# Performance work log

Hardware: AMD Instinct MI355X
Metric: run time of the kernel (lower is better)

## Reference

```python
import jax, jax.numpy as jnp
import numpy as np
import math

D, NH, NL, NP_ = 256, 8, 3, 4
BS, LQ = 32, 300
SHAPES = [(80, 80), (40, 40), (20, 20)]
LV = sum(h * w for h, w in SHAPES)  # 8400
DFF = 1024


def _offset_bias():
    # faithful to MSDeformableAttention._reset_parameters
    thetas = jnp.arange(NH, dtype=jnp.float32) * (2.0 * math.pi / NH)
    grid = jnp.stack([jnp.cos(thetas), jnp.sin(thetas)], -1)
    grid = grid / jnp.abs(grid).max(-1, keepdims=True)
    grid = jnp.tile(grid.reshape(NH, 1, 1, 2), (1, NL, NP_, 1))
    grid = grid * jnp.arange(1, NP_ + 1, dtype=jnp.float32).reshape(1, 1, -1, 1)
    return grid.reshape(-1)


def setup_inputs() -> dict:
    key = jax.random.key(0)
    ks = iter(jax.random.split(key, 64))
    rn = lambda shape, s=0.02: jax.random.normal(next(ks), shape, jnp.float32) * s
    z = lambda n: jnp.zeros((n,), jnp.float32)
    o = lambda n: jnp.ones((n,), jnp.float32)
    inp = {
        'tgt': jax.random.normal(next(ks), (BS, LQ, D), jnp.float32),
        'reference_points': jax.random.uniform(next(ks), (BS, LQ, NL, 2), jnp.float32),
        'memory': jax.random.normal(next(ks), (BS, LV, D), jnp.float32),
        'query_pos_embed': jax.random.normal(next(ks), (BS, LQ, D), jnp.float32),
        'memory_spatial_shapes': np.array(SHAPES, dtype=np.int64),
        'memory_level_start_index': np.array([0, 6400, 8000], dtype=np.int64),
        # self-attn
        'Wq': rn((D, D)), 'bq': z(D), 'Wk': rn((D, D)), 'bk': z(D),
        'Wv': rn((D, D)), 'bv': z(D), 'Wo': rn((D, D)), 'bo': z(D),
        'ln1_g': o(D), 'ln1_b': z(D),
        # deformable cross-attn
        'W_vproj': rn((D, D)), 'b_vproj': z(D),
        'W_off': rn((D, NH * NL * NP_ * 2), 0.001), 'b_off': _offset_bias(),
        'W_attn': rn((D, NH * NL * NP_)), 'b_attn': z(NH * NL * NP_),
        'W_out': rn((D, D)), 'b_out': z(D),
        'ln2_g': o(D), 'ln2_b': z(D),
        # FFN
        'W1': rn((D, DFF)), 'b1': z(DFF), 'W2': rn((DFF, D)), 'b2': z(D),
        'ln3_g': o(D), 'ln3_b': z(D),
    }
    return inp


def _ln(x, g, b):
    m = x.mean(-1, keepdims=True)
    v = ((x - m) ** 2).mean(-1, keepdims=True)
    return (x - m) / jnp.sqrt(v + 1e-5) * g + b


def _ms_deform(value, shapes, loc, aw):
    # value [bs,Lv,nh,c]; loc [bs,Lq,nh,NL,NP,2] in [0,1]; aw [bs,Lq,nh,NL,NP]
    bs, Lv, nh, c = value.shape
    Lq = loc.shape[1]
    npts = loc.shape[4]
    grids = 2.0 * loc - 1.0
    out = jnp.zeros((bs, nh, Lq, c), value.dtype)
    start = 0
    for lvl, (h, w) in enumerate(shapes):
        flat = value[:, start:start + h * w].transpose(0, 2, 1, 3)  # [bs,nh,hw,c]
        start += h * w
        g = grids[:, :, :, lvl].transpose(0, 2, 1, 3, 4).reshape(bs, nh, Lq * npts, 2)
        # align_corners=False pixel coords
        x = (g[..., 0] + 1.0) * (w / 2.0) - 0.5
        y = (g[..., 1] + 1.0) * (h / 2.0) - 0.5
        x0 = jnp.floor(x); y0 = jnp.floor(y)
        wx1 = x - x0; wy1 = y - y0
        samp = jnp.zeros((bs, nh, Lq * npts, c), value.dtype)
        for xi, yi, wgt in ((x0, y0, (1 - wx1) * (1 - wy1)),
                            (x0 + 1, y0, wx1 * (1 - wy1)),
                            (x0, y0 + 1, (1 - wx1) * wy1),
                            (x0 + 1, y0 + 1, wx1 * wy1)):
            valid = (xi >= 0) & (xi < w) & (yi >= 0) & (yi < h)
            idx = (jnp.clip(yi, 0, h - 1) * w + jnp.clip(xi, 0, w - 1)).astype(jnp.int32)
            idx = jnp.broadcast_to(idx[..., None], idx.shape + (c,))
            gv = jnp.take_along_axis(flat, idx, axis=2)  # [bs,nh,Lq*np,c]
            samp = samp + gv * (wgt * valid.astype(value.dtype))[..., None]
        samp = samp.reshape(bs, nh, Lq, npts, c)
        a = aw[:, :, :, lvl].transpose(0, 2, 1, 3)  # [bs,nh,Lq,np]
        out = out + (samp * a[..., None]).sum(3)
    return out.transpose(0, 2, 1, 3).reshape(bs, Lq, nh * c)


def reference(tgt, reference_points, memory, query_pos_embed,
              memory_spatial_shapes, memory_level_start_index,
              Wq, bq, Wk, bk, Wv, bv, Wo, bo, ln1_g, ln1_b,
              W_vproj, b_vproj, W_off, b_off, W_attn, b_attn, W_out, b_out,
              ln2_g, ln2_b, W1, b1, W2, b2, ln3_g, ln3_b):
    shapes = [(int(h), int(w)) for h, w in np.asarray(memory_spatial_shapes)]
    bs, Lq, d = tgt.shape
    hd = d // NH
    # --- self attention (dropout=eval identity, attn_mask=None) ---
    q = tgt + query_pos_embed
    qh = (q @ Wq + bq).reshape(bs, Lq, NH, hd)
    kh = (q @ Wk + bk).reshape(bs, Lq, NH, hd)
    vh = (tgt @ Wv + bv).reshape(bs, Lq, NH, hd)
    att = jax.nn.softmax(jnp.einsum('bqhd,bkhd->bhqk', qh, kh) / jnp.sqrt(jnp.float32(hd)), axis=-1)
    sa = jnp.einsum('bhqk,bkhd->bqhd', att, vh).reshape(bs, Lq, d) @ Wo + bo
    tgt = _ln(tgt + sa, ln1_g, ln1_b)
    # --- deformable cross attention ---
    qc = tgt + query_pos_embed
    value = (memory @ W_vproj + b_vproj).reshape(bs, -1, NH, hd)
    off = (qc @ W_off + b_off).reshape(bs, Lq, NH, NL, NP_, 2)
    aw = jax.nn.softmax((qc @ W_attn + b_attn).reshape(bs, Lq, NH, NL * NP_), axis=-1)
    aw = aw.reshape(bs, Lq, NH, NL, NP_)
    norm = jnp.array([[w, h] for h, w in shapes], jnp.float32)  # flip -> (w,h)
    loc = reference_points[:, :, None, :, None, :] + off / norm[None, None, None, :, None, :]
    ca = _ms_deform(value, shapes, loc, aw) @ W_out + b_out
    tgt = _ln(tgt + ca, ln2_g, ln2_b)
    # --- FFN ---
    h = jax.nn.relu(tgt @ W1 + b1) @ W2 + b2
    return _ln(tgt + h, ln3_g, ln3_b)
```

## Files before the change

### kernel.cpp

```cpp
#include <hip/hip_runtime.h>
#include <hip/hip_bf16.h>

#define D_      256
#define NH_     8
#define HD_     32
#define NL_     3
#define NP_4    4
#define BS_     32
#define LQ_     300
#define LV_     8400
#define DFF_    1024
#define NTOK    (BS_ * LQ_)
#define NVAL    (BS_ * LV_)

typedef __attribute__((ext_vector_type(8))) short bf16x8;
typedef __attribute__((ext_vector_type(4))) float f32x4;

__device__ inline unsigned short f2bf(float x) {
    union { float f; unsigned u; } v; v.f = x;
    unsigned r = v.u + 0x7FFFu + ((v.u >> 16) & 1u);
    return (unsigned short)(r >> 16);
}
__device__ inline float bf2f(unsigned short x) {
    union { unsigned u; float f; } v; v.u = ((unsigned)x) << 16;
    return v.f;
}

struct TrDesc { const float* W; unsigned short* Wt; int K; int N; };
struct TrPack { TrDesc d[10]; };

__global__ __launch_bounds__(256)
void tr_kernel(TrPack p) {
    TrDesc d = p.d[blockIdx.z];
    const int n0 = blockIdx.x * 32, k0 = blockIdx.y * 32;
    if (n0 >= d.N || k0 >= d.K) return;
    __shared__ float t[32][33];
    const int tx = threadIdx.x & 31, ty = threadIdx.x >> 5;
    #pragma unroll
    for (int i = 0; i < 4; ++i) {
        int k = k0 + ty + i * 8, n = n0 + tx;
        t[ty + i * 8][tx] = (k < d.K && n < d.N) ? d.W[(size_t)k * d.N + n] : 0.f;
    }
    __syncthreads();
    #pragma unroll
    for (int i = 0; i < 4; ++i) {
        int n = n0 + ty + i * 8, k = k0 + tx;
        if (n < d.N && k < d.K) d.Wt[(size_t)n * d.K + k] = f2bf(t[tx][ty + i * 8]);
    }
}

template <int AROWS, int KK, int TC, int AMODE, int CMODE>
__global__ __launch_bounds__(256, 2)
void gemm_wreg(const void* __restrict__ Ain, const float* __restrict__ A2,
               const unsigned short* __restrict__ Wt, const float* __restrict__ bias,
               void* __restrict__ Cout, int M, int N) {
    constexpr int KSTEPS = KK / 32;
    constexpr int RT = AROWS / 16;
    constexpr int LDK = KK + 8;
    constexpr int TPR = 256 / AROWS;
    constexpr int KSEG = KK / TPR;
    __shared__ unsigned short Alds[AROWS * LDK];

    const int tid = threadIdx.x;
    const int lane = tid & 63, w = tid >> 6;
    const int quad = lane >> 4, l16 = lane & 15;
    const int rowBase = blockIdx.y * AROWS;
    const int colW = blockIdx.x * (4 * TC * 16) + w * (TC * 16);

    bf16x8 wf[TC][KSTEPS];
    #pragma unroll
    for (int j = 0; j < TC; ++j) {
        int col = colW + j * 16 + l16;
        if (col > N - 1) col = N - 1;
        const unsigned short* wp = Wt + (size_t)col * KK;
        #pragma unroll
        for (int s = 0; s < KSTEPS; ++s)
            wf[j][s] = *(const bf16x8*)(wp + s * 32 + quad * 8);
    }

    {
        const int row = tid / TPR;
        const int ks = (tid % TPR) * KSEG;
        const size_t gbase = (size_t)(rowBase + row) * KK + ks;
        unsigned short* dst = &Alds[row * LDK + ks];
        if (AMODE == 2) {
            const int4* ap = (const int4*)((const unsigned short*)Ain + gbase);
            int4 wa[KSEG / 8];
            #pragma unroll
            for (int j = 0; j < KSEG / 8; ++j) wa[j] = ap[j];
            #pragma unroll
            for (int j = 0; j < KSEG / 8; ++j) *(int4*)(dst + j * 8) = wa[j];
        } else {
            const float4* ap = (const float4*)((const float*)Ain + gbase);
            float4 va[KSEG / 4];
            #pragma unroll
            for (int j = 0; j < KSEG / 4; ++j) va[j] = ap[j];
            if (AMODE == 1) {
                const float4* bp = (const float4*)(A2 + gbase);
                float4 vb[KSEG / 4];
                #pragma unroll
                for (int j = 0; j < KSEG / 4; ++j) vb[j] = bp[j];
                #pragma unroll
                for (int j = 0; j < KSEG / 4; ++j) {
                    va[j].x += vb[j].x; va[j].y += vb[j].y;
                    va[j].z += vb[j].z; va[j].w += vb[j].w;
                }
            }
            #pragma unroll
            for (int j = 0; j < KSEG / 4; ++j) {
                ushort4 s4;
                s4.x = f2bf(va[j].x); s4.y = f2bf(va[j].y);
                s4.z = f2bf(va[j].z); s4.w = f2bf(va[j].w);
                *(ushort4*)(dst + j * 4) = s4;
            }
        }
    }
    __syncthreads();

    f32x4 acc[RT][TC];
    #pragma unroll
    for (int rt = 0; rt < RT; ++rt)
        #pragma unroll
        for (int j = 0; j < TC; ++j)
            #pragma unroll
            for (int r = 0; r < 4; ++r) acc[rt][j][r] = 0.f;

    #pragma unroll
    for (int s = 0; s < KSTEPS; ++s) {
        bf16x8 af[RT];
        #pragma unroll
        for (int rt = 0; rt < RT; ++rt)
            af[rt] = *(const bf16x8*)&Alds[(rt * 16 + l16) * LDK + s * 32 + quad * 8];
        #pragma unroll
        for (int rt = 0; rt < RT; ++rt)
            #pragma unroll
            for (int j = 0; j < TC; ++j)
                acc[rt][j] = __builtin_amdgcn_mfma_f32_16x16x32_bf16(af[rt], wf[j][s], acc[rt][j], 0, 0, 0);
    }

    #pragma unroll
    for (int rt = 0; rt < RT; ++rt) {
        #pragma unroll
        for (int j = 0; j < TC; ++j) {
            int col = colW + j * 16 + l16;
            if (col >= N) continue;
            float bb = bias[col];
            #pragma unroll
            for (int r = 0; r < 4; ++r) {
                int row = rowBase + rt * 16 + quad * 4 + r;
                float c = acc[rt][j][r] + bb;
                if (CMODE == 1 || CMODE == 3) c = fmaxf(c, 0.f);
                if (CMODE >= 2)
                    ((unsigned short*)Cout)[(size_t)row * N + col] = f2bf(c);
                else
                    ((float*)Cout)[(size_t)row * N + col] = c;
            }
        }
    }
}

#define PS_STRIDE 344
__global__ __launch_bounds__(256)
void attn_mfma(const unsigned short* __restrict__ qh,
               const unsigned short* __restrict__ kh,
               const unsigned short* __restrict__ vh,
               float* __restrict__ out) {
    __shared__ unsigned short Ps[4 * 16 * PS_STRIDE];
    __shared__ unsigned short Vs[32 * PS_STRIDE];
    const int tid = threadIdx.x;
    const int bh = blockIdx.x >> 1, half_ = blockIdx.x & 1;
    const int b = bh >> 3, h = bh & 7;
    const int w = tid >> 6, lane = tid & 63;
    const int quad = lane >> 4, l16 = lane & 15;

    for (int i = tid; i < 4 * 16 * PS_STRIDE / 2; i += 256) ((unsigned*)Ps)[i] = 0u;

    const size_t hbase = ((size_t)b * LQ_) * D_ + h * HD_;
    for (int it = 0; it < 10; ++it) {
        int chunk = tid + 256 * it;
        int key = chunk >> 3, cc = (chunk & 7) * 4;
        ushort4 v = make_ushort4(0, 0, 0, 0);
        if (key < LQ_) v = *(const ushort4*)(vh + hbase + (size_t)key * D_ + cc);
        Vs[(cc + 0) * PS_STRIDE + key] = v.x;
        Vs[(cc + 1) * PS_STRIDE + key] = v.y;
        Vs[(cc + 2) * PS_STRIDE + key] = v.z;
        Vs[(cc + 3) * PS_STRIDE + key] = v.w;
    }
    __syncthreads();

    const unsigned short* qb = qh + hbase;
    const unsigned short* kb = kh + hbase;
    const float scale = 0.17677669529663687f;

    for (int qt = 10 * half_ + w; qt < 10 * half_ + 10 && qt < 19; qt += 4) {
        int rowq = qt * 16 + l16; if (rowq > LQ_ - 1) rowq = LQ_ - 1;
        bf16x8 aq = *(const bf16x8*)(qb + (size_t)rowq * D_ + quad * 8);

        f32x4 S[19];
        #pragma unroll
        for (int kt = 0; kt < 19; ++kt) {
            int rowk = kt * 16 + l16; if (rowk > LQ_ - 1) rowk = LQ_ - 1;
            bf16x8 bk = *(const bf16x8*)(kb + (size_t)rowk * D_ + quad * 8);
            f32x4 z; z[0] = z[1] = z[2] = z[3] = 0.f;
            S[kt] = __builtin_amdgcn_mfma_f32_16x16x32_bf16(aq, bk, z, 0, 0, 0);
        }
        float mrow[4] = {-1e30f, -1e30f, -1e30f, -1e30f};
        #pragma unroll
        for (int kt = 0; kt < 19; ++kt) {
            bool masked = (kt == 18) && (l16 >= 12);
            #pragma unroll
            for (int r = 0; r < 4; ++r) {
                float s = masked ? -1e30f : S[kt][r] * scale;
                S[kt][r] = s;
                mrow[r] = fmaxf(mrow[r], s);
            }
        }
        #pragma unroll
        for (int r = 0; r < 4; ++r)
            #pragma unroll
            for (int off = 1; off < 16; off <<= 1)
                mrow[r] = fmaxf(mrow[r], __shfl_xor(mrow[r], off));
        float psum[4] = {0.f, 0.f, 0.f, 0.f};
        #pragma unroll
        for (int kt = 0; kt < 19; ++kt)
            #pragma unroll
            for (int r = 0; r < 4; ++r) {
                float p = __expf(S[kt][r] - mrow[r]);
                S[kt][r] = p;
                psum[r] += p;
            }
        #pragma unroll
        for (int r = 0; r < 4; ++r)
            #pragma unroll
            for (int off = 1; off < 16; off <<= 1)
                psum[r] += __shfl_xor(psum[r], off);
        float linv[4];
        #pragma unroll
        for (int r = 0; r < 4; ++r) linv[r] = 1.f / psum[r];

        unsigned short* pw = Ps + w * (16 * PS_STRIDE);
        #pragma unroll
        for (int kt = 0; kt < 19; ++kt)
            #pragma unroll
            for (int r = 0; r < 4; ++r)
                pw[(quad * 4 + r) * PS_STRIDE + kt * 16 + l16] = f2bf(S[kt][r]);

        f32x4 o0, o1;
        #pragma unroll
        for (int r = 0; r < 4; ++r) { o0[r] = 0.f; o1[r] = 0.f; }
        #pragma unroll
        for (int ks = 0; ks < 10; ++ks) {
            bf16x8 ap = *(const bf16x8*)(pw + l16 * PS_STRIDE + ks * 32 + quad * 8);
            bf16x8 b0 = *(const bf16x8*)(Vs + l16 * PS_STRIDE + ks * 32 + quad * 8);
            bf16x8 b1 = *(const bf16x8*)(Vs + (16 + l16) * PS_STRIDE + ks * 32 + quad * 8);
            o0 = __builtin_amdgcn_mfma_f32_16x16x32_bf16(ap, b0, o0, 0, 0, 0);
            o1 = __builtin_amdgcn_mfma_f32_16x16x32_bf16(ap, b1, o1, 0, 0, 0);
        }
        #pragma unroll
        for (int r = 0; r < 4; ++r) {
            int q = qt * 16 + quad * 4 + r;
            if (q < LQ_) {
                size_t ob = ((size_t)b * LQ_ + q) * D_ + h * HD_;
                out[ob + l16]      = o0[r] * linv[r];
                out[ob + 16 + l16] = o1[r] * linv[r];
            }
        }
    }
}

__global__ __launch_bounds__(256)
void ln_kernel(const float* __restrict__ x, const float* __restrict__ r,
               const float* __restrict__ g, const float* __restrict__ bta,
               float* __restrict__ out) {
    const int tok = blockIdx.x;
    const int t = threadIdx.x;
    float v = x[(size_t)tok * D_ + t] + r[(size_t)tok * D_ + t];

    float s = v;
    #pragma unroll
    for (int i = 1; i < 64; i <<= 1) s += __shfl_xor(s, i);
    __shared__ float red1[4];
    if ((t & 63) == 0) red1[t >> 6] = s;
    __syncthreads();
    float mean = (red1[0] + red1[1] + red1[2] + red1[3]) * (1.0f / D_);

    float d = v - mean;
    float s2 = d * d;
    #pragma unroll
    for (int i = 1; i < 64; i <<= 1) s2 += __shfl_xor(s2, i);
    __shared__ float red2[4];
    if ((t & 63) == 0) red2[t >> 6] = s2;
    __syncthreads();
    float var = (red2[0] + red2[1] + red2[2] + red2[3]) * (1.0f / D_);

    out[(size_t)tok * D_ + t] = d * rsqrtf(var + 1e-5f) * g[t] + bta[t];
}

__global__ __launch_bounds__(256)
void deform_kernel(const unsigned short* __restrict__ value,
                   const float* __restrict__ off,
                   const float* __restrict__ awl,
                   const float* __restrict__ ref,
                   float* __restrict__ out) {
    const int lvl_hw[3]    = {80, 40, 20};
    const int lvl_start[3] = {0, 6400, 8000};
    const int gid = blockIdx.x * 16 + (threadIdx.x >> 4);
    const int c2  = (threadIdx.x & 15) * 2;
    const int h   = gid & 7;
    const int bq  = gid >> 3;
    const int b   = bq / LQ_;

    float lg[12];
    const float* ap = awl + (size_t)bq * 96 + h * 12;
    float m = -1e30f;
    #pragma unroll
    for (int j = 0; j < 12; ++j) { lg[j] = ap[j]; m = fmaxf(m, lg[j]); }
    float s = 0.f;
    #pragma unroll
    for (int j = 0; j < 12; ++j) { lg[j] = __expf(lg[j] - m); s += lg[j]; }
    const float inv = 1.0f / s;

    const float* op = off + (size_t)bq * 192 + h * 24;
    const float* rp = ref + (size_t)bq * 6;

    float accx = 0.f, accy = 0.f;
    #pragma unroll
    for (int l = 0; l < NL_; ++l) {
        const int W = lvl_hw[l], H = lvl_hw[l];
        const float fw = (float)W, fh = (float)H;
        const float rx = rp[l * 2 + 0], ry = rp[l * 2 + 1];
        const unsigned short* vbase =
            value + ((size_t)b * LV_ + lvl_start[l]) * D_ + h * HD_ + c2;
        #pragma unroll
        for (int p = 0; p < NP_4; ++p) {
            float ox = op[(l * 4 + p) * 2 + 0], oy = op[(l * 4 + p) * 2 + 1];
            float x = (rx + ox / fw) * fw - 0.5f;
            float y = (ry + oy / fh) * fh - 0.5f;
            float x0f = floorf(x), y0f = floorf(y);
            float wx = x - x0f, wy = y - y0f;
            int x0 = (int)x0f, y0 = (int)y0f;
            float a = lg[l * 4 + p] * inv;
            const float cw[4] = {a * (1.f - wx) * (1.f - wy), a * wx * (1.f - wy),
                                 a * (1.f - wx) * wy,         a * wx * wy};
            const int cx[4] = {x0, x0 + 1, x0,     x0 + 1};
            const int cy[4] = {y0, y0,     y0 + 1, y0 + 1};
            #pragma unroll
            for (int cor = 0; cor < 4; ++cor) {
                int xi = cx[cor], yi = cy[cor];
                if (xi < 0 || xi >= W || yi < 0 || yi >= H) continue;
                unsigned v = *(const unsigned*)(vbase + (size_t)(yi * W + xi) * D_);
                accx += cw[cor] * bf2f((unsigned short)(v & 0xFFFFu));
                accy += cw[cor] * bf2f((unsigned short)(v >> 16));
            }
        }
    }
    float2 o2; o2.x = accx; o2.y = accy;
    *(float2*)(out + (size_t)bq * D_ + h * HD_ + c2) = o2;
}

extern "C" void kernel_launch(void* const* d_in, const int* in_sizes, int n_in,
                              void* d_out, int out_size, void* d_ws, size_t ws_size,
                              hipStream_t stream) {
    const float* tgt   = (const float*)d_in[0];
    const float* refpt = (const float*)d_in[1];
    const float* mem   = (const float*)d_in[2];
    const float* qpos  = (const float*)d_in[3];
    const float* Wq = (const float*)d_in[6],  *bq = (const float*)d_in[7];
    const float* Wk = (const float*)d_in[8],  *bk = (const float*)d_in[9];
    const float* Wv = (const float*)d_in[10], *bv = (const float*)d_in[11];
    const float* Wo = (const float*)d_in[12], *bo = (const float*)d_in[13];
    const float* ln1_g = (const float*)d_in[14], *ln1_b = (const float*)d_in[15];
    const float* W_vproj = (const float*)d_in[16], *b_vproj = (const float*)d_in[17];
    const float* W_off  = (const float*)d_in[18], *b_off  = (const float*)d_in[19];
    const float* W_attn = (const float*)d_in[20], *b_attn = (const float*)d_in[21];
    const float* W_out  = (const float*)d_in[22], *b_out  = (const float*)d_in[23];
    const float* ln2_g = (const float*)d_in[24], *ln2_b = (const float*)d_in[25];
    const float* W1 = (const float*)d_in[26], *b1 = (const float*)d_in[27];
    const float* W2 = (const float*)d_in[28], *b2 = (const float*)d_in[29];
    const float* ln3_g = (const float*)d_in[30], *ln3_b = (const float*)d_in[31];
    float* out = (float*)d_out;

    char* p = (char*)d_ws;
    const size_t TOKD = (size_t)NTOK * D_;
    float* buf_attn = (float*)p; p += TOKD * 4;
    float* buf_tmp  = (float*)p; p += TOKD * 4;
    float* buf_t1   = (float*)p; p += TOKD * 4;
    float* buf_t2   = (float*)p; p += TOKD * 4;
    unsigned short* buf_qh = (unsigned short*)p; p += TOKD * 2;
    unsigned short* buf_kh = (unsigned short*)p; p += TOKD * 2;
    unsigned short* buf_vh = (unsigned short*)p; p += TOKD * 2;
    float* buf_off  = (float*)p; p += (size_t)NTOK * 192 * 4;
    float* buf_awl  = (float*)p; p += (size_t)NTOK * 96 * 4;
    unsigned short* wt_q   = (unsigned short*)p; p += 65536 * 2;
    unsigned short* wt_k   = (unsigned short*)p; p += 65536 * 2;
    unsigned short* wt_v   = (unsigned short*)p; p += 65536 * 2;
    unsigned short* wt_o   = (unsigned short*)p; p += 65536 * 2;
    unsigned short* wt_vp  = (unsigned short*)p; p += 65536 * 2;
    unsigned short* wt_off = (unsigned short*)p; p += 49152 * 2;
    unsigned short* wt_awl = (unsigned short*)p; p += 24576 * 2;
    unsigned short* wt_out = (unsigned short*)p; p += 65536 * 2;
    unsigned short* wt_1   = (unsigned short*)p; p += (size_t)262144 * 2;
    unsigned short* wt_2   = (unsigned short*)p; p += (size_t)262144 * 2;
    unsigned short* buf_value = (unsigned short*)p;
    unsigned short* buf_ffnb  = (unsigned short*)p;

    TrPack pk;
    pk.d[0] = {Wq,      wt_q,   256, 256};
    pk.d[1] = {Wk,      wt_k,   256, 256};
    pk.d[2] = {Wv,      wt_v,   256, 256};
    pk.d[3] = {Wo,      wt_o,   256, 256};
    pk.d[4] = {W_vproj, wt_vp,  256, 256};
    pk.d[5] = {W_off,   wt_off, 256, 192};
    pk.d[6] = {W_attn,  wt_awl, 256, 96};
    pk.d[7] = {W_out,   wt_out, 256, 256};
    pk.d[8] = {W1,      wt_1,   256, 1024};
    pk.d[9] = {W2,      wt_2,   1024, 256};
    tr_kernel<<<dim3(32, 32, 10), 256, 0, stream>>>(pk);

    gemm_wreg<32, 256, 4, 1, 2><<<dim3(1, NTOK / 32), 256, 0, stream>>>(
        tgt, qpos, wt_q, bq, buf_qh, NTOK, 256);
    gemm_wreg<32, 256, 4, 1, 2><<<dim3(1, NTOK / 32), 256, 0, stream>>>(
        tgt, qpos, wt_k, bk, buf_kh, NTOK, 256);
    gemm_wreg<32, 256, 4, 0, 2><<<dim3(1, NTOK / 32), 256, 0, stream>>>(
        tgt, nullptr, wt_v, bv, buf_vh, NTOK, 256);
    attn_mfma<<<BS_ * NH_ * 2, 256, 0, stream>>>(buf_qh, buf_kh, buf_vh, buf_attn);
    gemm_wreg<32, 256, 4, 0, 0><<<dim3(1, NTOK / 32), 256, 0, stream>>>(
        buf_attn, nullptr, wt_o, bo, buf_tmp, NTOK, 256);
    ln_kernel<<<NTOK, 256, 0, stream>>>(tgt, buf_tmp, ln1_g, ln1_b, buf_t1);

    gemm_wreg<64, 256, 4, 0, 2><<<dim3(1, NVAL / 64), 256, 0, stream>>>(
        mem, nullptr, wt_vp, b_vproj, buf_value, NVAL, 256);
    gemm_wreg<32, 256, 4, 1, 0><<<dim3(1, NTOK / 32), 256, 0, stream>>>(
        buf_t1, qpos, wt_off, b_off, buf_off, NTOK, 192);
    gemm_wreg<32, 256, 4, 1, 0><<<dim3(1, NTOK / 32), 256, 0, stream>>>(
        buf_t1, qpos, wt_awl, b_attn, buf_awl, NTOK, 96);
    deform_kernel<<<(BS_ * LQ_ * NH_) / 16, 256, 0, stream>>>(
        buf_value, buf_off, buf_awl, refpt, buf_attn);
    gemm_wreg<32, 256, 4, 0, 0><<<dim3(1, NTOK / 32), 256, 0, stream>>>(
        buf_attn, nullptr, wt_out, b_out, buf_tmp, NTOK, 256);
    ln_kernel<<<NTOK, 256, 0, stream>>>(buf_t1, buf_tmp, ln2_g, ln2_b, buf_t2);

    gemm_wreg<32, 256, 4, 0, 3><<<dim3(4, NTOK / 32), 256, 0, stream>>>(
        buf_t2, nullptr, wt_1, b1, buf_ffnb, NTOK, DFF_);
    gemm_wreg<16, 1024, 1, 2, 0><<<dim3(4, NTOK / 16), 256, 0, stream>>>(
        buf_ffnb, nullptr, wt_2, b2, buf_tmp, NTOK, 256);
    ln_kernel<<<NTOK, 256, 0, stream>>>(buf_t2, buf_tmp, ln3_g, ln3_b, out);
}
```

Before: 833.4 us.

## Replace register-resident weight GEMM with LDS-staged output-stationary tiled GEMM

Replaces the GEMM that held each warp's weight fragments in registers with an output-stationary GEMM that stages both the A tile and the weight tile in LDS, optionally over K chunks, and uses a 2D warp grid. Tile shapes are retuned per call: wider column splits for the small-token GEMMs, 128x128 tiles for the large value projection, and a K-chunked FFN2. The intent is to cut per-block weight loads into registers and improve A/B reuse for large-M GEMMs. In exchange it adds more LDS traffic and synchronisation, drops to one block per CU via launch bounds, and removes the column bounds check.

```diff
diff --git a/kernel.cpp b/kernel.cpp
--- a/kernel.cpp
+++ b/kernel.cpp
@@ -49,105 +49,103 @@
     }
 }
 
-template <int AROWS, int KK, int TC, int AMODE, int CMODE>
-__global__ __launch_bounds__(256, 2)
-void gemm_wreg(const void* __restrict__ Ain, const float* __restrict__ A2,
-               const unsigned short* __restrict__ Wt, const float* __restrict__ bias,
-               void* __restrict__ Cout, int M, int N) {
-    constexpr int KSTEPS = KK / 32;
-    constexpr int RT = AROWS / 16;
-    constexpr int LDK = KK + 8;
-    constexpr int TPR = 256 / AROWS;
-    constexpr int KSEG = KK / TPR;
-    __shared__ unsigned short Alds[AROWS * LDK];
-
-    const int tid = threadIdx.x;
-    const int lane = tid & 63, w = tid >> 6;
+template <int ROWS, int COLS, int KK, int KC, int WR, int WC, int AMODE, int CMODE>
+__global__ __launch_bounds__(256, 1)
+void gemm_os(const void* __restrict__ Ain, const float* __restrict__ A2,
+             const unsigned short* __restrict__ Wt, const float* __restrict__ bias,
+             void* __restrict__ Cout, int M, int N) {
+    constexpr int LDK = KC + 8;
+    constexpr int NC = KK / KC;
+    constexpr int KS = KC / 32;
+    constexpr int WROWS = ROWS / WR, WCOLS = COLS / WC;
+    constexpr int RT = WROWS / 16, TC = WCOLS / 16;
+    __shared__ unsigned short Alds[ROWS * LDK];
+    __shared__ unsigned short Blds[COLS * LDK];
+
+    const int tid = threadIdx.x, lane = tid & 63, w = tid >> 6;
     const int quad = lane >> 4, l16 = lane & 15;
-    const int rowBase = blockIdx.y * AROWS;
-    const int colW = blockIdx.x * (4 * TC * 16) + w * (TC * 16);
-
-    bf16x8 wf[TC][KSTEPS];
-    #pragma unroll
-    for (int j = 0; j < TC; ++j) {
-        int col = colW + j * 16 + l16;
-        if (col > N - 1) col = N - 1;
-        const unsigned short* wp = Wt + (size_t)col * KK;
-        #pragma unroll
-        for (int s = 0; s < KSTEPS; ++s)
-            wf[j][s] = *(const bf16x8*)(wp + s * 32 + quad * 8);
-    }
-
-    {
-        const int row = tid / TPR;
-        const int ks = (tid % TPR) * KSEG;
-        const size_t gbase = (size_t)(rowBase + row) * KK + ks;
-        unsigned short* dst = &Alds[row * LDK + ks];
-        if (AMODE == 2) {
-            const int4* ap = (const int4*)((const unsigned short*)Ain + gbase);
-            int4 wa[KSEG / 8];
-            #pragma unroll
-            for (int j = 0; j < KSEG / 8; ++j) wa[j] = ap[j];
-            #pragma unroll
-            for (int j = 0; j < KSEG / 8; ++j) *(int4*)(dst + j * 8) = wa[j];
-        } else {
-            const float4* ap = (const float4*)((const float*)Ain + gbase);
-            float4 va[KSEG / 4];
-            #pragma unroll
-            for (int j = 0; j < KSEG / 4; ++j) va[j] = ap[j];
-            if (AMODE == 1) {
-                const float4* bp = (const float4*)(A2 + gbase);
-                float4 vb[KSEG / 4];
+    const int wr = w / WC, wc = w % WC;
+    const int rowBase = blockIdx.y * ROWS;
+    const int colBase = blockIdx.x * COLS;
+
+    f32x4 acc[RT][TC];
+    #pragma unroll
+    for (int rt = 0; rt < RT; ++rt)
+        #pragma unroll
+        for (int j = 0; j < TC; ++j)
+            #pragma unroll
+            for (int r = 0; r < 4; ++r) acc[rt][j][r] = 0.f;
+
+    for (int ch = 0; ch < NC; ++ch) {
+        if (NC > 1) __syncthreads();
+        {
+            constexpr int CNT = ROWS * KC / 1024;
+            if (AMODE == 2) {
+                constexpr int CNT2 = ROWS * KC / 2048;
                 #pragma unroll
-                for (int j = 0; j < KSEG / 4; ++j) vb[j] = bp[j];
+                for (int i = 0; i < CNT2; ++i) {
+                    int idx = i * 256 + tid;
+                    int row = idx / (KC / 8), kofs = (idx % (KC / 8)) * 8;
+                    int4 v = *(const int4*)((const unsigned short*)Ain +
+                              (size_t)(rowBase + row) * KK + ch * KC + kofs);
+                    *(int4*)&Alds[row * LDK + kofs] = v;
+                }
+            } else {
                 #pragma unroll
-                for (int j = 0; j < KSEG / 4; ++j) {
-                    va[j].x += vb[j].x; va[j].y += vb[j].y;
-                    va[j].z += vb[j].z; va[j].w += vb[j].w;
+                for (int i = 0; i < CNT; ++i) {
+                    int idx = i * 256 + tid;
+                    int row = idx / (KC / 4), kofs = (idx % (KC / 4)) * 4;
+                    size_t g = (size_t)(rowBase + row) * KK + ch * KC + kofs;
+                    float4 a = *(const float4*)((const float*)Ain + g);
+                    if (AMODE == 1) {
+                        float4 b = *(const float4*)(A2 + g);
+                        a.x += b.x; a.y += b.y; a.z += b.z; a.w += b.w;
+                    }
+                    ushort4 s4;
+                    s4.x = f2bf(a.x); s4.y = f2bf(a.y);
+                    s4.z = f2bf(a.z); s4.w = f2bf(a.w);
+                    *(ushort4*)&Alds[row * LDK + kofs] = s4;
                 }
             }
-            #pragma unroll
-            for (int j = 0; j < KSEG / 4; ++j) {
-                ushort4 s4;
-                s4.x = f2bf(va[j].x); s4.y = f2bf(va[j].y);
-                s4.z = f2bf(va[j].z); s4.w = f2bf(va[j].w);
-                *(ushort4*)(dst + j * 4) = s4;
-            }
-        }
-    }
-    __syncthreads();
-
-    f32x4 acc[RT][TC];
-    #pragma unroll
-    for (int rt = 0; rt < RT; ++rt)
-        #pragma unroll
-        for (int j = 0; j < TC; ++j)
-            #pragma unroll
-            for (int r = 0; r < 4; ++r) acc[rt][j][r] = 0.f;
-
-    #pragma unroll
-    for (int s = 0; s < KSTEPS; ++s) {
-        bf16x8 af[RT];
-        #pragma unroll
-        for (int rt = 0; rt < RT; ++rt)
-            af[rt] = *(const bf16x8*)&Alds[(rt * 16 + l16) * LDK + s * 32 + quad * 8];
-        #pragma unroll
-        for (int rt = 0; rt < RT; ++rt)
+        }
+        {
+            constexpr int CNT = COLS * KC / 2048;
+            #pragma unroll
+            for (int i = 0; i < CNT; ++i) {
+                int idx = i * 256 + tid;
+                int col = idx / (KC / 8), kofs = (idx % (KC / 8)) * 8;
+                int4 v = *(const int4*)(Wt + (size_t)(colBase + col) * KK + ch * KC + kofs);
+                *(int4*)&Blds[col * LDK + kofs] = v;
+            }
+        }
+        __syncthreads();
+
+        #pragma unroll
+        for (int s = 0; s < KS; ++s) {
+            bf16x8 af[RT], bf[TC];
+            #pragma unroll
+            for (int rt = 0; rt < RT; ++rt)
+                af[rt] = *(const bf16x8*)&Alds[(wr * WROWS + rt * 16 + l16) * LDK + s * 32 + quad * 8];
             #pragma unroll
             for (int j = 0; j < TC; ++j)
-                acc[rt][j] = __builtin_amdgcn_mfma_f32_16x16x32_bf16(af[rt], wf[j][s], acc[rt][j], 0, 0, 0);
+                bf[j] = *(const bf16x8*)&Blds[(wc * WCOLS + j * 16 + l16) * LDK + s * 32 + quad * 8];
+            #pragma unroll
+            for (int rt = 0; rt < RT; ++rt)
+                #pragma unroll
+                for (int j = 0; j < TC; ++j)
+                    acc[rt][j] = __builtin_amdgcn_mfma_f32_16x16x32_bf16(af[rt], bf[j], acc[rt][j], 0, 0, 0);
+        }
     }
 
     #pragma unroll
     for (int rt = 0; rt < RT; ++rt) {
         #pragma unroll
         for (int j = 0; j < TC; ++j) {
-            int col = colW + j * 16 + l16;
-            if (col >= N) continue;
+            int col = colBase + wc * WCOLS + j * 16 + l16;
             float bb = bias[col];
             #pragma unroll
             for (int r = 0; r < 4; ++r) {
-                int row = rowBase + rt * 16 + quad * 4 + r;
+                int row = rowBase + wr * WROWS + rt * 16 + quad * 4 + r;
                 float c = acc[rt][j][r] + bb;
                 if (CMODE == 1 || CMODE == 3) c = fmaxf(c, 0.f);
                 if (CMODE >= 2)
@@ -417,32 +415,32 @@
     pk.d[9] = {W2,      wt_2,   1024, 256};
     tr_kernel<<<dim3(32, 32, 10), 256, 0, stream>>>(pk);
 
-    gemm_wreg<32, 256, 4, 1, 2><<<dim3(1, NTOK / 32), 256, 0, stream>>>(
+    gemm_os<32, 128, 256, 256, 1, 4, 1, 2><<<dim3(2, NTOK / 32), 256, 0, stream>>>(
         tgt, qpos, wt_q, bq, buf_qh, NTOK, 256);
-    gemm_wreg<32, 256, 4, 1, 2><<<dim3(1, NTOK / 32), 256, 0, stream>>>(
+    gemm_os<32, 128, 256, 256, 1, 4, 1, 2><<<dim3(2, NTOK / 32), 256, 0, stream>>>(
         tgt, qpos, wt_k, bk, buf_kh, NTOK, 256);
-    gemm_wreg<32, 256, 4, 0, 2><<<dim3(1, NTOK / 32), 256, 0, stream>>>(
+    gemm_os<32, 128, 256, 256, 1, 4, 0, 2><<<dim3(2, NTOK / 32), 256, 0, stream>>>(
         tgt, nullptr, wt_v, bv, buf_vh, NTOK, 256);
     attn_mfma<<<BS_ * NH_ * 2, 256, 0, stream>>>(buf_qh, buf_kh, buf_vh, buf_attn);
-    gemm_wreg<32, 256, 4, 0, 0><<<dim3(1, NTOK / 32), 256, 0, stream>>>(
+    gemm_os<32, 128, 256, 256, 1, 4, 0, 0><<<dim3(2, NTOK / 32), 256, 0, stream>>>(
         buf_attn, nullptr, wt_o, bo, buf_tmp, NTOK, 256);
     ln_kernel<<<NTOK, 256, 0, stream>>>(tgt, buf_tmp, ln1_g, ln1_b, buf_t1);
 
-    gemm_wreg<64, 256, 4, 0, 2><<<dim3(1, NVAL / 64), 256, 0, stream>>>(
+    gemm_os<128, 128, 256, 256, 2, 2, 0, 2><<<dim3(2, NVAL / 128), 256, 0, stream>>>(
         mem, nullptr, wt_vp, b_vproj, buf_value, NVAL, 256);
-    gemm_wreg<32, 256, 4, 1, 0><<<dim3(1, NTOK / 32), 256, 0, stream>>>(
+    gemm_os<32, 192, 256, 256, 1, 4, 1, 0><<<dim3(1, NTOK / 32), 256, 0, stream>>>(
         buf_t1, qpos, wt_off, b_off, buf_off, NTOK, 192);
-    gemm_wreg<32, 256, 4, 1, 0><<<dim3(1, NTOK / 32), 256, 0, stream>>>(
+    gemm_os<32, 96, 256, 256, 2, 2, 1, 0><<<dim3(1, NTOK / 32), 256, 0, stream>>>(
         buf_t1, qpos, wt_awl, b_attn, buf_awl, NTOK, 96);
     deform_kernel<<<(BS_ * LQ_ * NH_) / 16, 256, 0, stream>>>(
         buf_value, buf_off, buf_awl, refpt, buf_attn);
-    gemm_wreg<32, 256, 4, 0, 0><<<dim3(1, NTOK / 32), 256, 0, stream>>>(
+    gemm_os<32, 128, 256, 256, 1, 4, 0, 0><<<dim3(2, NTOK / 32), 256, 0, stream>>>(
         buf_attn, nullptr, wt_out, b_out, buf_tmp, NTOK, 256);
     ln_kernel<<<NTOK, 256, 0, stream>>>(buf_t1, buf_tmp, ln2_g, ln2_b, buf_t2);
 
-    gemm_wreg<32, 256, 4, 0, 3><<<dim3(4, NTOK / 32), 256, 0, stream>>>(
+    gemm_os<32, 128, 256, 256, 1, 4, 0, 3><<<dim3(8, NTOK / 32), 256, 0, stream>>>(
         buf_t2, nullptr, wt_1, b1, buf_ffnb, NTOK, DFF_);
-    gemm_wreg<16, 1024, 1, 2, 0><<<dim3(4, NTOK / 16), 256, 0, stream>>>(
+    gemm_os<32, 64, 1024, 512, 1, 4, 2, 0><<<dim3(4, NTOK / 32), 256, 0, stream>>>(
         buf_ffnb, nullptr, wt_2, b2, buf_tmp, NTOK, 256);
     ln_kernel<<<NTOK, 256, 0, stream>>>(buf_t2, buf_tmp, ln3_g, ln3_b, out);
 }
```

After: 781.7 us. -6.2%, faster.
